# Optimization experiments

Measured on AMD Instinct MI355X. Metric: run time of the kernel, lower is better.

Reference implementation:

```python
import jax, jax.numpy as jnp
import numpy as np

B, C, P, H, W, S = 4, 256, 128, 56, 56, 5
EPS = 1e-5


def setup_inputs() -> dict:
    key = jax.random.key(0)
    ks = jax.random.split(key, 6)
    return {
        "x": jax.random.normal(ks[0], (B, C, H, W), jnp.float32),
        "Wt": jax.random.normal(ks[1], (P, C), jnp.float32) * 0.05,
        "Wp": jax.random.normal(ks[2], (P, C), jnp.float32) * 0.05,
        "Wg": jax.random.normal(ks[3], (S, P, C), jnp.float32) * 0.05,
        "W1": jax.random.normal(ks[4], (S, C, P), jnp.float32) * 0.05,
        "W2": jax.random.normal(ks[5], (S, C, P), jnp.float32) * 0.05,
        "gamma": jnp.ones((S, C), jnp.float32),
        "beta": jnp.zeros((S, C), jnp.float32),
    }


def _batchnorm(o, g, b):
    # training-mode BN over (batch, spatial); o: [b, C, n]
    mean = o.mean(axis=(0, 2), keepdims=True)
    var = ((o - mean) ** 2).mean(axis=(0, 2), keepdims=True)
    return (o - mean) * jax.lax.rsqrt(var + EPS) * g[None, :, None] + b[None, :, None]


def reference(x, Wt, Wp, Wg, W1, W2, gamma, beta):
    b, c, h, w = x.shape
    n = h * w
    xf = x.reshape(b, c, n)
    # 1x1 conv projections == channel matmuls
    t = jax.nn.relu(jnp.einsum('pc,bcn->bpn', Wt, xf))  # is_norm branch uses relu
    p = jax.nn.relu(jnp.einsum('pc,bcn->bpn', Wp, xf))
    att = jnp.einsum('bpi,bpj->bij', t, p)              # [b, n, n] affinity
    att = 0.5 * (att + jnp.swapaxes(att, 1, 2))         # is_sys symmetrization
    d = att.sum(axis=2)                                  # degree [b, n]
    d_safe = jnp.where(d != 0, d, 1.0)
    d_inv = jnp.where(d != 0, jax.lax.rsqrt(d_safe), 0.0)
    att = att * d_inv[:, None, :] * d_inv[:, :, None]    # D^-1/2 A D^-1/2
    out = xf
    for s in range(S):  # fixed small stage count
        g = jnp.einsum('pc,bcn->bpn', Wg[s], out)        # [b, P, n]
        ag = jnp.einsum('bij,bpj->bpi', att, g)          # att @ g over spatial
        o = jnp.einsum('cp,bpn->bcn', W1[s], ag) + jnp.einsum('cp,bpn->bcn', W2[s], g)
        out = _batchnorm(o, gamma[s], beta[s]) + out     # BN + residual
    return out.reshape(b, c, h, w)
```

## Files before the change

### kernel.cpp

```cpp
#include <hip/hip_runtime.h>

#define VMC(n) asm volatile("s_waitcnt vmcnt(" #n ")" ::: "memory")
#define LGKM0() asm volatile("s_waitcnt lgkmcnt(0)" ::: "memory")

namespace {

constexpr int Bc = 4;
constexpr int Cc = 256;
constexpr int Pc = 128;
constexpr int NcT = 3136;
constexpr int Np = 3200;
constexpr int Sc = 5;
constexpr int KSn = 5;
constexpr int KCH = 640;
constexpr float EPSc = 1e-5f;

typedef __attribute__((ext_vector_type(8))) short bf16x8;
typedef __attribute__((ext_vector_type(4))) float f32x4;
typedef __attribute__((ext_vector_type(8))) unsigned short u16x8;
typedef __attribute__((ext_vector_type(4))) unsigned short u16x4;

__device__ inline float bf2f(unsigned short u) {
    return __uint_as_float(((unsigned)u) << 16);
}
__device__ inline unsigned short f2bf(float f) {
    unsigned u = __float_as_uint(f);
    return (unsigned short)((u + 0x7FFFu + ((u >> 16) & 1u)) >> 16);
}

struct GP {
    const unsigned short* A; int lda; long aB; long aSl;
    const unsigned short* Bw; int ldb; long bB; long bSl;
    const unsigned short* A2; int lda2; long aB2;
    const unsigned short* B2; int ldb2; long bB2;
    int K; int K2; int nsl; int kchunk;
    unsigned short* outSM; int ldsm; long smB; long smSlice;
    unsigned short* outCM; long cmB;
    float* ps; float* ps2;
    const float* bnsc; const float* bnsh;
    const float* dinv;
    const unsigned short* oin;
    float* resid;
};

template <int MT, int EPI, int CMOUT, bool SPLITK, int BNSTAT, bool FUSEBN,
          bool XORM, bool DUALK>
__global__ __launch_bounds__(256) void mgemm(GP p)
{
    constexpr int TBA = MT * 64 * 2;
    constexpr int TBB = 128 * 64 * 2;
    constexpr int BUF = TBA + TBB;
    constexpr int OTB = MT * 132 * 4;
    constexpr int LDSZ = (4 * BUF > OTB + 2048) ? 4 * BUF : (OTB + 2048);
    __shared__ __align__(16) char lds[LDSZ];

    int b, kstart;
    long smOff;
    if (SPLITK) {
        b = blockIdx.z & 3;
        int ks = blockIdx.z >> 2;
        kstart = ks * p.kchunk;
        smOff = (long)ks * p.smSlice;
    } else {
        b = blockIdx.z; kstart = 0; smOff = 0;
    }
    const int n0 = blockIdx.x * 128;
    const int m0 = blockIdx.y * MT;
    const int tid = threadIdx.x;
    const int w = tid >> 6, l = tid & 63;

    const unsigned short* Ab = p.A + (size_t)b * p.aB + (size_t)m0 * p.lda;
    const unsigned short* Bb = p.Bw + (size_t)b * p.bB + (size_t)n0 * p.ldb;

    const int srow8 = tid >> 3;
    const int sgran = tid & 7;
    const int sswz = (sgran ^ (srow8 & 7)) * 8;
    constexpr int AR = MT / 32;

    constexpr int WC = (MT == 128) ? 2 : 4;
    constexpr int NB = 128 / WC / 16;
    const int wr = w / WC, wc = w % WC;

    f32x4 acc[4][NB] = {};

    float4 dvv[4];
    if constexpr (DUALK) {
#pragma unroll
        for (int r = 0; r < 4; ++r) {
            float4 v = *(const float4*)(p.dinv + (size_t)b * Np + m0 +
                                        wr * 64 + r * 16 + (l >> 4) * 4);
            v.x *= 0.5f; v.y *= 0.5f; v.z *= 0.5f; v.w *= 0.5f;
            dvv[r] = v;
        }
    }

    auto stage1 = [&](int buf, int sl, int k0) {
        char* base = lds + buf * BUF;
        const unsigned short* As = Ab + (size_t)sl * p.aSl + k0 + sswz;
#pragma unroll
        for (int j = 0; j < AR; ++j)
            __builtin_amdgcn_global_load_lds(
                (const __attribute__((address_space(1))) void*)
                    (As + (size_t)(j * 32 + srow8) * p.lda),
                (__attribute__((address_space(3))) void*)(base + j * 4096 + tid * 16),
                16, 0, 0);
        const unsigned short* Bs = Bb + (size_t)sl * p.bSl + k0 + sswz;
#pragma unroll
        for (int j = 0; j < 4; ++j)
            __builtin_amdgcn_global_load_lds(
                (const __attribute__((address_space(1))) void*)
                    (Bs + (size_t)(j * 32 + srow8) * p.ldb),
                (__attribute__((address_space(3))) void*)(base + TBA + j * 4096 + tid * 16),
                16, 0, 0);
    };

    auto stageB1 = [&](int buf, int k0) {
        char* base = lds + buf * BUF + TBA;
        const unsigned short* Bs = Bb + k0 + sswz;
#pragma unroll
        for (int j = 0; j < 4; ++j)
            __builtin_amdgcn_global_load_lds(
                (const __attribute__((address_space(1))) void*)
                    (Bs + (size_t)(j * 32 + srow8) * p.ldb),
                (__attribute__((address_space(3))) void*)(base + j * 4096 + tid * 16),
                16, 0, 0);
    };

    auto compute = [&](int buf) {
        const char* base = lds + buf * BUF;
        const int lo = l & 15, gq = l >> 4;
#pragma unroll
        for (int kh = 0; kh < 2; ++kh) {
            const int lg = kh * 4 + gq;
            bf16x8 bf[NB];
#pragma unroll
            for (int c = 0; c < NB; ++c) {
                int brow = wc * (16 * NB) + c * 16 + lo;
                bf[c] = *(const bf16x8*)(base + TBA + brow * 128 +
                                         ((lg ^ (brow & 7)) << 4));
            }
#pragma unroll
            for (int r = 0; r < 4; ++r) {
                int arow = wr * 64 + r * 16 + lo;
                bf16x8 af = *(const bf16x8*)(base + arow * 128 +
                                             ((lg ^ (arow & 7)) << 4));
#pragma unroll
                for (int c = 0; c < NB; ++c)
                    acc[r][c] = __builtin_amdgcn_mfma_f32_16x16x32_bf16(
                        af, bf[c], acc[r][c], 0, 0, 0);
            }
        }
    };

    if constexpr (FUSEBN) {
        struct FB {
            u16x8 ov[AR]; float4 r0[AR], r1[AR];
            float4 s0, s1, h0, h1; int k0;
        };
        FB fA, fB;
        auto fbIssue = [&](FB& f, int k0) {
            f.k0 = k0;
            f.s0 = *(const float4*)(p.bnsc + k0 + sgran * 8);
            f.s1 = *(const float4*)(p.bnsc + k0 + sgran * 8 + 4);
            f.h0 = *(const float4*)(p.bnsh + k0 + sgran * 8);
            f.h1 = *(const float4*)(p.bnsh + k0 + sgran * 8 + 4);
#pragma unroll
            for (int j = 0; j < AR; ++j) {
                size_t off = ((size_t)b * Np + (m0 + j * 32 + srow8)) * 256 +
                             k0 + sgran * 8;
                f.ov[j] = *(const u16x8*)(p.oin + off);
                f.r0[j] = *(const float4*)(p.resid + off);
                f.r1[j] = *(const float4*)(p.resid + off + 4);
            }
        };
        auto fbFin = [&](FB& f, int buf) {
            char* base = lds + buf * BUF;
#pragma unroll
            for (int j = 0; j < AR; ++j) {
                int row = j * 32 + srow8;
                int n = m0 + row;
                size_t off = ((size_t)b * Np + n) * 256 + f.k0 + sgran * 8;
                bool real = (n < NcT);
                float fu[8];
                fu[0] = real ? f.r0[j].x + fmaf(bf2f(f.ov[j][0]), f.s0.x, f.h0.x) : 0.f;
                fu[1] = real ? f.r0[j].y + fmaf(bf2f(f.ov[j][1]), f.s0.y, f.h0.y) : 0.f;
                fu[2] = real ? f.r0[j].z + fmaf(bf2f(f.ov[j][2]), f.s0.z, f.h0.z) : 0.f;
                fu[3] = real ? f.r0[j].w + fmaf(bf2f(f.ov[j][3]), f.s0.w, f.h0.w) : 0.f;
                fu[4] = real ? f.r1[j].x + fmaf(bf2f(f.ov[j][4]), f.s1.x, f.h1.x) : 0.f;
                fu[5] = real ? f.r1[j].y + fmaf(bf2f(f.ov[j][5]), f.s1.y, f.h1.y) : 0.f;
                fu[6] = real ? f.r1[j].z + fmaf(bf2f(f.ov[j][6]), f.s1.z, f.h1.z) : 0.f;
                fu[7] = real ? f.r1[j].w + fmaf(bf2f(f.ov[j][7]), f.s1.w, f.h1.w) : 0.f;
                float4 w0, w1;
                w0.x = fu[0]; w0.y = fu[1]; w0.z = fu[2]; w0.w = fu[3];
                w1.x = fu[4]; w1.y = fu[5]; w1.z = fu[6]; w1.w = fu[7];
                *(float4*)(p.resid + off) = w0;
                *(float4*)(p.resid + off + 4) = w1;
                u16x8 hv;
#pragma unroll
                for (int i = 0; i < 8; ++i) hv[i] = f2bf(fu[i]);
                *(u16x8*)(base + row * 128 + ((sgran ^ (row & 7)) << 4)) = hv;
            }
        };

        fbIssue(fA, kstart);        stageB1(0, kstart);
        fbIssue(fB, kstart + 64);   stageB1(1, kstart + 64);
        VMC(14);
        fbFin(fA, 0);
        fbIssue(fA, kstart + 128);  stageB1(2, kstart + 128);
        LGKM0();
        __builtin_amdgcn_s_barrier();
        __builtin_amdgcn_sched_barrier(0);
        compute(0);
        VMC(18);
        fbFin(fB, 1);
        fbIssue(fB, kstart + 192);  stageB1(3, kstart + 192);
        LGKM0();
        __builtin_amdgcn_s_barrier();
        __builtin_amdgcn_sched_barrier(0);
        compute(1);
        VMC(18);
        fbFin(fA, 2);
        LGKM0();
        __builtin_amdgcn_s_barrier();
        __builtin_amdgcn_sched_barrier(0);
        compute(2);
        VMC(4);
        fbFin(fB, 3);
        LGKM0();
        __builtin_amdgcn_s_barrier();
        __builtin_amdgcn_sched_barrier(0);
        compute(3);
        __syncthreads();
    } else {
        const int nsteps1 = (SPLITK ? p.kchunk : p.K) >> 6;
        const int spl2 = DUALK ? (p.K2 >> 6) : 0;
        const int loop1 = p.nsl * nsteps1;
        const int tot = loop1 + spl2;

        const unsigned short* Ab2 = DUALK ?
            (p.A2 + (size_t)b * p.aB2 + (size_t)m0 * p.lda2) : nullptr;
        const unsigned short* Bb2 = DUALK ?
            (p.B2 + (size_t)b * p.bB2 + (size_t)n0 * p.ldb2) : nullptr;
        auto stage2 = [&](int buf, int k0) {
            if constexpr (DUALK) {
                char* base = lds + buf * BUF;
                const unsigned short* As = Ab2 + k0 + sswz;
#pragma unroll
                for (int j = 0; j < AR; ++j)
                    __builtin_amdgcn_global_load_lds(
                        (const __attribute__((address_space(1))) void*)
                            (As + (size_t)(j * 32 + srow8) * p.lda2),
                        (__attribute__((address_space(3))) void*)(base + j * 4096 + tid * 16),
                        16, 0, 0);
                const unsigned short* Bs = Bb2 + k0 + sswz;
#pragma unroll
                for (int j = 0; j < 4; ++j)
                    __builtin_amdgcn_global_load_lds(
                        (const __attribute__((address_space(1))) void*)
                            (Bs + (size_t)(j * 32 + srow8) * p.ldb2),
                        (__attribute__((address_space(3))) void*)(base + TBA + j * 4096 + tid * 16),
                        16, 0, 0);
            }
        };

        auto stage_g = [&](int buf, int g) {
            if (g < loop1) {
                int sl = g / nsteps1;
                int st = g - sl * nsteps1;
                stage1(buf, sl, kstart + (st << 6));
            } else {
                stage2(buf, (g - loop1) << 6);
            }
        };

        stage_g(0, 0);
        if (1 < tot) stage_g(1, 1);
        if (2 < tot) stage_g(2, 2);
        for (int gs = 0; gs < tot; ++gs) {
            if constexpr (MT == 64) {
                if (gs + 2 < tot) VMC(12);
                else if (gs + 1 < tot) VMC(6);
                else VMC(0);
            } else {
                if (gs + 2 < tot) VMC(16);
                else if (gs + 1 < tot) VMC(8);
                else VMC(0);
            }
            __builtin_amdgcn_s_barrier();
            __builtin_amdgcn_sched_barrier(0);
            if (gs + 3 < tot) stage_g((gs + 3) & 3, gs + 3);
            compute(gs & 3);
            if constexpr (DUALK) {
                if (gs == loop1 - 1) {
#pragma unroll
                    for (int r = 0; r < 4; ++r) {
#pragma unroll
                        for (int c = 0; c < NB; ++c) {
                            acc[r][c][0] *= dvv[r].x;
                            acc[r][c][1] *= dvv[r].y;
                            acc[r][c][2] *= dvv[r].z;
                            acc[r][c][3] *= dvv[r].w;
                        }
                    }
                }
            }
        }
        __syncthreads();
    }

    float* ot = (float*)lds;
    {
        const int lo = l & 15, gq = l >> 4;
#pragma unroll
        for (int r = 0; r < 4; ++r)
#pragma unroll
            for (int c = 0; c < NB; ++c)
#pragma unroll
                for (int j = 0; j < 4; ++j) {
                    float v = acc[r][c][j];
                    if (EPI == 1) v = fmaxf(v, 0.f);
                    ot[(wr * 64 + r * 16 + gq * 4 + j) * 132 +
                       wc * (16 * NB) + c * 16 + lo] = v;
                }
    }
    __syncthreads();

    {
        constexpr int TPR = 256 / MT;
        const int r = tid / TPR;
        const int c0 = (tid % TPR) * (MT / 2);
        const int m0s = XORM ? (m0 ^ 128) : m0;
        unsigned short* dst = p.outSM + (size_t)b * p.smB + smOff +
                              (size_t)(m0s + r) * p.ldsm + n0 + c0;
#pragma unroll
        for (int k = 0; k < MT / 16; ++k) {
            u16x8 o;
#pragma unroll
            for (int j = 0; j < 8; ++j) o[j] = f2bf(ot[r * 132 + c0 + 8 * k + j]);
            *(u16x8*)(dst + 8 * k) = o;
        }
    }

    if (CMOUT) {
        const int c = tid >> 1, r0 = (tid & 1) * (MT / 2);
        const float* dv = p.dinv + (size_t)b * Np + m0 + r0;
        unsigned short* dst = p.outCM + (size_t)b * p.cmB +
                              (size_t)(n0 + c) * Np + m0 + r0;
#pragma unroll
        for (int k = 0; k < MT / 16; ++k) {
            u16x8 o;
#pragma unroll
            for (int j = 0; j < 8; ++j) {
                float v = ot[(r0 + 8 * k + j) * 132 + c];
                if (CMOUT == 2) v *= dv[8 * k + j];
                o[j] = f2bf(v);
            }
            *(u16x8*)(dst + 8 * k) = o;
        }
    }

    if (BNSTAT) {
        float* p1 = (float*)(lds + OTB);
        float* p2 = p1 + 256;
        const int col = tid & 127, half = tid >> 7;
        float s = 0.f, s2 = 0.f;
#pragma unroll
        for (int i = 0; i < MT / 2; ++i) {
            float v = ot[(half * (MT / 2) + i) * 132 + col];
            s += v;
            if (BNSTAT == 2) s2 = fmaf(v, v, s2);
        }
        p1[half * 128 + col] = s;
        if (BNSTAT == 2) p2[half * 128 + col] = s2;
        __syncthreads();
        if (tid < 128) {
            float aa = p1[tid] + p1[128 + tid];
            size_t slot = ((size_t)b * gridDim.y + blockIdx.y) * 256 + n0 + tid;
            p.ps[slot] = aa;
            if (BNSTAT == 2) p.ps2[slot] = p2[tid] + p2[128 + tid];
        }
    }
}

__global__ __launch_bounds__(256) void prep_k(
    const float* __restrict__ x, const float* __restrict__ Wt,
    const float* __restrict__ Wp, const float* __restrict__ Wg,
    const float* __restrict__ W1, const float* __restrict__ W2,
    unsigned short* __restrict__ Wcomb, unsigned short* __restrict__ Wgh,
    unsigned short* __restrict__ W1h, unsigned short* __restrict__ W2h,
    float* __restrict__ out_sm, unsigned short* __restrict__ outh)
{
    __shared__ float tb[64][65];
    int item = blockIdx.x;
    int t = threadIdx.x;
    if (item < 544) {
        size_t e = ((size_t)item * 256 + t) * 4;
        const float* src; unsigned short* dst;
        if (e < 32768)       { src = Wt + e;           dst = Wcomb + e; }
        else if (e < 65536)  { src = Wp + (e - 32768); dst = Wcomb + e; }
        else if (e < 229376) { size_t o = e - 65536;  src = Wg + o; dst = Wgh + o; }
        else if (e < 393216) { size_t o = e - 229376; src = W1 + o; dst = W1h + o; }
        else                 { size_t o = e - 393216; src = W2 + o; dst = W2h + o; }
        float4 v = *(const float4*)src;
        u16x4 t4;
        t4[0] = f2bf(v.x); t4[1] = f2bf(v.y); t4[2] = f2bf(v.z); t4[3] = f2bf(v.w);
        *(u16x4*)dst = t4;
        return;
    }
    int it = item - 544;
    int nx = it % 50, cy = (it / 50) % 4, b = it / 200;
    int c0 = cy * 64, n0 = nx * 64;
    const bool pad = (n0 >= NcT);
    if (!pad) {
        int ci = t >> 2, nb = (t & 3) * 16;
        const float* src = x + ((size_t)b * Cc + c0 + ci) * NcT + n0 + nb;
#pragma unroll
        for (int k = 0; k < 4; ++k) {
            float4 v = *(const float4*)(src + 4 * k);
            tb[ci][nb + 4 * k + 0] = v.x; tb[ci][nb + 4 * k + 1] = v.y;
            tb[ci][nb + 4 * k + 2] = v.z; tb[ci][nb + 4 * k + 3] = v.w;
        }
    }
    __syncthreads();
    int r = t >> 2, cb = (t & 3) * 16;
    size_t off = ((size_t)b * Np + n0 + r) * 256 + c0 + cb;
    float vv[16];
#pragma unroll
    for (int j = 0; j < 16; ++j) vv[j] = pad ? 0.f : tb[cb + j][r];
    float* dst = out_sm + off;
#pragma unroll
    for (int k = 0; k < 4; ++k) {
        float4 v; v.x = vv[4*k]; v.y = vv[4*k+1]; v.z = vv[4*k+2]; v.w = vv[4*k+3];
        *(float4*)(dst + 4 * k) = v;
    }
    u16x8 h1, h2;
#pragma unroll
    for (int j = 0; j < 8; ++j) { h1[j] = f2bf(vv[j]); h2[j] = f2bf(vv[8 + j]); }
    unsigned short* dh = outh + off;
    *(u16x8*)dh = h1;
    *(u16x8*)(dh + 8) = h2;
}

__global__ __launch_bounds__(256) void dinv_k(
    const unsigned short* __restrict__ U, const float* __restrict__ rp,
    float* __restrict__ dinv)
{
    __shared__ float rsl[256];
    int b = blockIdx.y, tid = threadIdx.x;
    float s = 0.f;
    for (int j = 0; j < 25; ++j) s += rp[((size_t)b * 25 + j) * 256 + tid];
    rsl[tid ^ 128] = s;
    __syncthreads();
    int i = blockIdx.x * 256 + tid;
    if (i < Np) {
        const unsigned short* row = U + ((size_t)b * Np + i) * 256;
        float acc = 0.f;
        for (int q0 = 0; q0 < 256; q0 += 8) {
            u16x8 v = *(const u16x8*)(row + q0);
#pragma unroll
            for (int j = 0; j < 8; ++j) acc = fmaf(bf2f(v[j]), rsl[q0 + j], acc);
        }
        float d = 0.5f * acc;
        dinv[(size_t)b * Np + i] = d > 0.f ? rsqrtf(d) : 0.f;
    }
}

__global__ __launch_bounds__(256) void bnfin_k(
    const float* __restrict__ ps, const float* __restrict__ ps2,
    const float* __restrict__ gamma, const float* __restrict__ beta,
    float* __restrict__ scale, float* __restrict__ shift)
{
    __shared__ float l1[256], l2[256];
    int t = threadIdx.x;
    int c = blockIdx.x * 16 + (t & 15);
    int gl = t >> 4;
    float a = 0.f, a2 = 0.f;
    for (int g = gl; g < 100; g += 16) {
        a += ps[(size_t)g * 256 + c];
        a2 += ps2[(size_t)g * 256 + c];
    }
    l1[t] = a; l2[t] = a2;
    __syncthreads();
    if (gl == 0) {
#pragma unroll
        for (int j = 1; j < 16; ++j) {
            a += l1[j * 16 + (t & 15)];
            a2 += l2[j * 16 + (t & 15)];
        }
        const float inv = 1.f / (float)(Bc * NcT);
        float mean = a * inv;
        float var = a2 * inv - mean * mean;
        float sc = gamma[c] * rsqrtf(var + EPSc);
        scale[c] = sc;
        shift[c] = beta[c] - mean * sc;
    }
}

__global__ __launch_bounds__(256) void xpoutbn_k(
    const float* __restrict__ out_sm, const unsigned short* __restrict__ oin,
    const float* __restrict__ scale, const float* __restrict__ shift,
    float* __restrict__ outp)
{
    __shared__ float tb[64][65];
    __shared__ float lsc[64], lsh[64];
    int b = blockIdx.z, c0 = blockIdx.y * 64, n0 = blockIdx.x * 64;
    int t = threadIdx.x;
    if (t < 64) { lsc[t] = scale[c0 + t]; lsh[t] = shift[c0 + t]; }
    __syncthreads();
    {
        int r = t >> 2, cb = (t & 3) * 16;
        size_t off = ((size_t)b * Np + n0 + r) * 256 + c0 + cb;
#pragma unroll
        for (int k = 0; k < 2; ++k) {
            float4 a0 = *(const float4*)(out_sm + off + 8 * k);
            float4 a1 = *(const float4*)(out_sm + off + 8 * k + 4);
            u16x8 ov = *(const u16x8*)(oin + off + 8 * k);
            tb[r][cb + 8*k + 0] = a0.x + fmaf(bf2f(ov[0]), lsc[cb + 8*k + 0], lsh[cb + 8*k + 0]);
            tb[r][cb + 8*k + 1] = a0.y + fmaf(bf2f(ov[1]), lsc[cb + 8*k + 1], lsh[cb + 8*k + 1]);
            tb[r][cb + 8*k + 2] = a0.z + fmaf(bf2f(ov[2]), lsc[cb + 8*k + 2], lsh[cb + 8*k + 2]);
            tb[r][cb + 8*k + 3] = a0.w + fmaf(bf2f(ov[3]), lsc[cb + 8*k + 3], lsh[cb + 8*k + 3]);
            tb[r][cb + 8*k + 4] = a1.x + fmaf(bf2f(ov[4]), lsc[cb + 8*k + 4], lsh[cb + 8*k + 4]);
            tb[r][cb + 8*k + 5] = a1.y + fmaf(bf2f(ov[5]), lsc[cb + 8*k + 5], lsh[cb + 8*k + 5]);
            tb[r][cb + 8*k + 6] = a1.z + fmaf(bf2f(ov[6]), lsc[cb + 8*k + 6], lsh[cb + 8*k + 6]);
            tb[r][cb + 8*k + 7] = a1.w + fmaf(bf2f(ov[7]), lsc[cb + 8*k + 7], lsh[cb + 8*k + 7]);
        }
    }
    __syncthreads();
    {
        int c = t >> 2, rb = (t & 3) * 16;
        float vv[16];
#pragma unroll
        for (int j = 0; j < 16; ++j) vv[j] = tb[rb + j][c];
        float* dst = outp + ((size_t)b * Cc + c0 + c) * NcT + n0 + rb;
#pragma unroll
        for (int k = 0; k < 4; ++k) {
            float4 v; v.x = vv[4*k]; v.y = vv[4*k+1]; v.z = vv[4*k+2]; v.w = vv[4*k+3];
            *(float4*)(dst + 4 * k) = v;
        }
    }
}

}

extern "C" void kernel_launch(void* const* d_in, const int* in_sizes, int n_in,
                              void* d_out, int out_size, void* d_ws, size_t ws_size,
                              hipStream_t stream) {
    const float* x     = (const float*)d_in[0];
    const float* Wt    = (const float*)d_in[1];
    const float* Wp    = (const float*)d_in[2];
    const float* Wg    = (const float*)d_in[3];
    const float* W1    = (const float*)d_in[4];
    const float* W2    = (const float*)d_in[5];
    const float* gamma = (const float*)d_in[6];
    const float* beta  = (const float*)d_in[7];

    char* p = (char*)d_ws;
    auto alloc = [&](size_t bytes) { char* r = p; p += (bytes + 255) & ~(size_t)255; return r; };
    float*          out_sm = (float*)         alloc((size_t)Bc * Np * 256 * 4);
    unsigned short* outh   = (unsigned short*)alloc((size_t)Bc * Np * 256 * 2);
    unsigned short* U_sm   = (unsigned short*)alloc((size_t)Bc * Np * 256 * 2);
    unsigned short* U_cm   = (unsigned short*)alloc((size_t)Bc * 256 * Np * 2);
    unsigned short* g_sm   = (unsigned short*)alloc((size_t)Bc * Np * Pc * 2);
    unsigned short* g_cmd  = (unsigned short*)alloc((size_t)Bc * Pc * Np * 2);
    unsigned short* o_sm   = (unsigned short*)alloc((size_t)Bc * Np * 256 * 2);
    unsigned short* Cpart  = (unsigned short*)alloc((size_t)KSn * Bc * 256 * Pc * 2);
    unsigned short* WMb    = (unsigned short*)alloc((size_t)Bc * Cc * 256 * 2);
    unsigned short* Wcomb  = (unsigned short*)alloc((size_t)Cc * Cc * 2);
    unsigned short* Wgh    = (unsigned short*)alloc((size_t)Sc * Pc * Cc * 2);
    unsigned short* W1h    = (unsigned short*)alloc((size_t)Sc * Cc * Pc * 2);
    unsigned short* W2h    = (unsigned short*)alloc((size_t)Sc * Cc * Pc * 2);
    float*          rp     = (float*)         alloc((size_t)100 * 256 * 4);
    float*          dinv   = (float*)         alloc((size_t)Bc * Np * 4);
    float*          ps     = (float*)         alloc((size_t)100 * 256 * 4);
    float*          ps2    = (float*)         alloc((size_t)100 * 256 * 4);
    float*          scale  = (float*)         alloc(256 * 4);
    float*          shiftb = (float*)         alloc(256 * 4);

    const long NpC = (long)Np * 256;
    dim3 blk(256);

    prep_k<<<1344, blk, 0, stream>>>(x, Wt, Wp, Wg, W1, W2,
                                     Wcomb, Wgh, W1h, W2h, out_sm, outh);

    {
        GP g{};
        g.A = outh; g.lda = 256; g.aB = NpC; g.aSl = 0;
        g.Bw = Wcomb; g.ldb = 256; g.bB = 0; g.bSl = 0;
        g.K = 256; g.nsl = 1;
        g.outSM = U_sm; g.ldsm = 256; g.smB = NpC; g.smSlice = 0;
        g.outCM = U_cm; g.cmB = (long)256 * Np;
        g.ps = rp;
        mgemm<128, 1, 1, false, 1, false, false, false>
            <<<dim3(2, 25, Bc), blk, 0, stream>>>(g);
    }

    dinv_k<<<dim3(13, Bc), blk, 0, stream>>>(U_sm, rp, dinv);

    for (int s = 0; s < Sc; ++s) {
        {
            GP g{};
            g.A = outh; g.lda = 256; g.aB = NpC; g.aSl = 0;
            g.Bw = Wgh + (size_t)s * Pc * Cc; g.ldb = 256; g.bB = 0; g.bSl = 0;
            g.K = 256; g.nsl = 1;
            g.outSM = g_sm; g.ldsm = 128; g.smB = (long)Np * 128; g.smSlice = 0;
            g.outCM = g_cmd; g.cmB = (long)Pc * Np;
            g.dinv = dinv;
            g.oin = o_sm; g.bnsc = scale; g.bnsh = shiftb; g.resid = out_sm;
            if (s == 0)
                mgemm<64, 0, 2, false, 0, false, false, false>
                    <<<dim3(1, 50, Bc), blk, 0, stream>>>(g);
            else
                mgemm<64, 0, 2, false, 0, true, false, false>
                    <<<dim3(1, 50, Bc), blk, 0, stream>>>(g);
        }
        {
            GP g{};
            g.A = U_cm; g.lda = Np; g.aB = (long)256 * Np; g.aSl = 0;
            g.Bw = g_cmd; g.ldb = Np; g.bB = (long)Pc * Np; g.bSl = 0;
            g.K = Np; g.kchunk = KCH; g.nsl = 1;
            g.outSM = Cpart; g.ldsm = 128; g.smB = (long)256 * Pc;
            g.smSlice = (long)Bc * 256 * Pc;
            mgemm<64, 0, 0, true, 0, false, true, false>
                <<<dim3(1, 4, KSn * Bc), blk, 0, stream>>>(g);
        }
        {
            GP g{};
            g.A = W1h + (size_t)s * Cc * Pc; g.lda = 128; g.aB = 0; g.aSl = 0;
            g.Bw = Cpart; g.ldb = 128; g.bB = (long)256 * Pc;
            g.bSl = (long)Bc * 256 * Pc;
            g.K = 128; g.nsl = KSn;
            g.outSM = WMb; g.ldsm = 256; g.smB = (long)Cc * 256; g.smSlice = 0;
            mgemm<64, 0, 0, false, 0, false, false, false>
                <<<dim3(2, 4, Bc), blk, 0, stream>>>(g);
        }
        {
            GP g{};
            g.A = U_sm; g.lda = 256; g.aB = NpC; g.aSl = 0;
            g.Bw = WMb; g.ldb = 256; g.bB = (long)Cc * 256; g.bSl = 0;
            g.K = 256; g.nsl = 1;
            g.A2 = g_sm; g.lda2 = 128; g.aB2 = (long)Np * 128;
            g.B2 = W2h + (size_t)s * Cc * Pc; g.ldb2 = 128; g.bB2 = 0;
            g.K2 = 128;
            g.outSM = o_sm; g.ldsm = 256; g.smB = NpC; g.smSlice = 0;
            g.ps = ps; g.ps2 = ps2;
            g.dinv = dinv;
            mgemm<128, 0, 0, false, 2, false, false, true>
                <<<dim3(2, 25, Bc), blk, 0, stream>>>(g);
        }
        bnfin_k<<<16, blk, 0, stream>>>(ps, ps2, gamma + s * Cc, beta + s * Cc,
                                        scale, shiftb);
    }

    xpoutbn_k<<<dim3(49, 4, Bc), blk, 0, stream>>>(out_sm, o_sm, scale, shiftb,
                                                   (float*)d_out);
}
```

Before: 250.5 us.

## Fuse per-stage GEMM chain into one persistent kernel with atomic flag barriers

The five per-stage launches (g projection, split-K att·g, W1 mix, dual-K output GEMM, BN finalize) are replaced by one 200-block kernel per stage. The GEMM bodies become device functions that take explicit block indices, and phases are ordered by global atomic counters with release/acquire semantics and sleep-polling. The aim is to remove launch gaps and tail drain between the dependent GEMMs. The cost is spin-wait latency and a 128 KB LDS footprint that allows only one block per CU. The scheme also depends on all 200 blocks being co-resident; a bounded spin guard avoids hangs but could silently break ordering if it ever trips.

```diff
diff --git a/kernel.cpp b/kernel.cpp
--- a/kernel.cpp
+++ b/kernel.cpp
@@ -43,29 +43,44 @@
     float* resid;
 };
 
+__device__ inline void signal_flag(unsigned* f) {
+    __syncthreads();
+    if (threadIdx.x == 0)
+        __hip_atomic_fetch_add(f, 1u, __ATOMIC_RELEASE, __HIP_MEMORY_SCOPE_AGENT);
+}
+__device__ inline void wait_flag(unsigned* f, unsigned target) {
+    if (threadIdx.x == 0) {
+        int guard = 0;
+        while (__hip_atomic_load(f, __ATOMIC_ACQUIRE,
+                                 __HIP_MEMORY_SCOPE_AGENT) < target) {
+            __builtin_amdgcn_s_sleep(8);
+            if (++guard > (1 << 20)) break;
+        }
+    }
+    __syncthreads();
+}
+
 template <int MT, int EPI, int CMOUT, bool SPLITK, int BNSTAT, bool FUSEBN,
           bool XORM, bool DUALK>
-__global__ __launch_bounds__(256) void mgemm(GP p)
+__device__ void gemm_body(char* lds, int bx, int by, int bz, int MY, const GP& p)
 {
     constexpr int TBA = MT * 64 * 2;
     constexpr int TBB = 128 * 64 * 2;
     constexpr int BUF = TBA + TBB;
     constexpr int OTB = MT * 132 * 4;
-    constexpr int LDSZ = (4 * BUF > OTB + 2048) ? 4 * BUF : (OTB + 2048);
-    __shared__ __align__(16) char lds[LDSZ];
 
     int b, kstart;
     long smOff;
     if (SPLITK) {
-        b = blockIdx.z & 3;
-        int ks = blockIdx.z >> 2;
+        b = bz & 3;
+        int ks = bz >> 2;
         kstart = ks * p.kchunk;
         smOff = (long)ks * p.smSlice;
     } else {
-        b = blockIdx.z; kstart = 0; smOff = 0;
-    }
-    const int n0 = blockIdx.x * 128;
-    const int m0 = blockIdx.y * MT;
+        b = bz; kstart = 0; smOff = 0;
+    }
+    const int n0 = bx * 128;
+    const int m0 = by * MT;
     const int tid = threadIdx.x;
     const int w = tid >> 6, l = tid & 63;
 
@@ -375,10 +390,100 @@
         __syncthreads();
         if (tid < 128) {
             float aa = p1[tid] + p1[128 + tid];
-            size_t slot = ((size_t)b * gridDim.y + blockIdx.y) * 256 + n0 + tid;
+            size_t slot = ((size_t)b * MY + by) * 256 + n0 + tid;
             p.ps[slot] = aa;
             if (BNSTAT == 2) p.ps2[slot] = p2[tid] + p2[128 + tid];
         }
+    }
+    __syncthreads();
+}
+
+__device__ void bnfin_body(char* ldsb, int bid,
+                           const float* __restrict__ ps,
+                           const float* __restrict__ ps2,
+                           const float* __restrict__ gamma,
+                           const float* __restrict__ beta,
+                           float* __restrict__ scale, float* __restrict__ shift)
+{
+    float* l1 = (float*)ldsb;
+    float* l2 = l1 + 256;
+    int t = threadIdx.x;
+    int c = bid * 16 + (t & 15);
+    int gl = t >> 4;
+    float a = 0.f, a2 = 0.f;
+    for (int g = gl; g < 100; g += 16) {
+        a += ps[(size_t)g * 256 + c];
+        a2 += ps2[(size_t)g * 256 + c];
+    }
+    l1[t] = a; l2[t] = a2;
+    __syncthreads();
+    if (gl == 0) {
+#pragma unroll
+        for (int j = 1; j < 16; ++j) {
+            a += l1[j * 16 + (t & 15)];
+            a2 += l2[j * 16 + (t & 15)];
+        }
+        const float inv = 1.f / (float)(Bc * NcT);
+        float mean = a * inv;
+        float var = a2 * inv - mean * mean;
+        float sc = gamma[c] * rsqrtf(var + EPSc);
+        scale[c] = sc;
+        shift[c] = beta[c] - mean * sc;
+    }
+}
+
+template <int MT, int EPI, int CMOUT, bool SPLITK, int BNSTAT, bool FUSEBN,
+          bool XORM, bool DUALK>
+__global__ __launch_bounds__(256) void mgemm_g(GP p)
+{
+    constexpr int TBA = MT * 64 * 2;
+    constexpr int BUF = TBA + 128 * 64 * 2;
+    constexpr int OTB = MT * 132 * 4;
+    constexpr int LDSZ = (4 * BUF > OTB + 2048) ? 4 * BUF : (OTB + 2048);
+    __shared__ __align__(16) char lds[LDSZ];
+    gemm_body<MT, EPI, CMOUT, SPLITK, BNSTAT, FUSEBN, XORM, DUALK>(
+        lds, blockIdx.x, blockIdx.y, blockIdx.z, (int)gridDim.y, p);
+}
+
+struct SP {
+    GP g, abt, wm, o;
+    const float* ps; const float* ps2;
+    const float* gammap; const float* betap;
+    float* scale; float* shiftb;
+    unsigned* flags;
+};
+
+template <bool FIRST>
+__global__ __launch_bounds__(256) void stage_k(SP sp)
+{
+    __shared__ __align__(16) char lds[131072];
+    const int bid = blockIdx.x;
+
+    gemm_body<64, 0, 2, false, 0, (FIRST ? false : true), false, false>(
+        lds, 0, bid % 50, bid / 50, 50, sp.g);
+    signal_flag(&sp.flags[0]);
+
+    if (bid < 80) {
+        wait_flag(&sp.flags[0], 200);
+        gemm_body<64, 0, 0, true, 0, false, true, false>(
+            lds, 0, bid % 4, bid / 4, 4, sp.abt);
+        signal_flag(&sp.flags[1]);
+    }
+    if (bid < 32) {
+        wait_flag(&sp.flags[1], 80);
+        gemm_body<64, 0, 0, false, 0, false, false, false>(
+            lds, bid % 2, (bid / 2) % 4, bid / 8, 4, sp.wm);
+        signal_flag(&sp.flags[2]);
+    }
+    wait_flag(&sp.flags[2], 32);
+    gemm_body<128, 0, 0, false, 2, false, false, true>(
+        lds, bid % 2, (bid / 2) % 25, bid / 50, 25, sp.o);
+    signal_flag(&sp.flags[3]);
+
+    if (bid < 16) {
+        wait_flag(&sp.flags[3], 200);
+        bnfin_body(lds, bid, sp.ps, sp.ps2, sp.gammap, sp.betap,
+                   sp.scale, sp.shiftb);
     }
 }
 
@@ -465,37 +570,6 @@
     }
 }
 
-__global__ __launch_bounds__(256) void bnfin_k(
-    const float* __restrict__ ps, const float* __restrict__ ps2,
-    const float* __restrict__ gamma, const float* __restrict__ beta,
-    float* __restrict__ scale, float* __restrict__ shift)
-{
-    __shared__ float l1[256], l2[256];
-    int t = threadIdx.x;
-    int c = blockIdx.x * 16 + (t & 15);
-    int gl = t >> 4;
-    float a = 0.f, a2 = 0.f;
-    for (int g = gl; g < 100; g += 16) {
-        a += ps[(size_t)g * 256 + c];
-        a2 += ps2[(size_t)g * 256 + c];
-    }
-    l1[t] = a; l2[t] = a2;
-    __syncthreads();
-    if (gl == 0) {
-#pragma unroll
-        for (int j = 1; j < 16; ++j) {
-            a += l1[j * 16 + (t & 15)];
-            a2 += l2[j * 16 + (t & 15)];
-        }
-        const float inv = 1.f / (float)(Bc * NcT);
-        float mean = a * inv;
-        float var = a2 * inv - mean * mean;
-        float sc = gamma[c] * rsqrtf(var + EPSc);
-        scale[c] = sc;
-        shift[c] = beta[c] - mean * sc;
-    }
-}
-
 __global__ __launch_bounds__(256) void xpoutbn_k(
     const float* __restrict__ out_sm, const unsigned short* __restrict__ oin,
     const float* __restrict__ scale, const float* __restrict__ shift,
@@ -575,9 +649,12 @@
     float*          ps2    = (float*)         alloc((size_t)100 * 256 * 4);
     float*          scale  = (float*)         alloc(256 * 4);
     float*          shiftb = (float*)         alloc(256 * 4);
+    unsigned*       flags  = (unsigned*)      alloc(Sc * 4 * sizeof(unsigned));
 
     const long NpC = (long)Np * 256;
     dim3 blk(256);
+
+    hipMemsetAsync(flags, 0, Sc * 4 * sizeof(unsigned), stream);
 
     prep_k<<<1344, blk, 0, stream>>>(x, Wt, Wp, Wg, W1, W2,
                                      Wcomb, Wgh, W1h, W2h, out_sm, outh);
@@ -590,65 +667,48 @@
         g.outSM = U_sm; g.ldsm = 256; g.smB = NpC; g.smSlice = 0;
         g.outCM = U_cm; g.cmB = (long)256 * Np;
         g.ps = rp;
-        mgemm<128, 1, 1, false, 1, false, false, false>
+        mgemm_g<128, 1, 1, false, 1, false, false, false>
             <<<dim3(2, 25, Bc), blk, 0, stream>>>(g);
     }
 
     dinv_k<<<dim3(13, Bc), blk, 0, stream>>>(U_sm, rp, dinv);
 
     for (int s = 0; s < Sc; ++s) {
-        {
-            GP g{};
-            g.A = outh; g.lda = 256; g.aB = NpC; g.aSl = 0;
-            g.Bw = Wgh + (size_t)s * Pc * Cc; g.ldb = 256; g.bB = 0; g.bSl = 0;
-            g.K = 256; g.nsl = 1;
-            g.outSM = g_sm; g.ldsm = 128; g.smB = (long)Np * 128; g.smSlice = 0;
-            g.outCM = g_cmd; g.cmB = (long)Pc * Np;
-            g.dinv = dinv;
-            g.oin = o_sm; g.bnsc = scale; g.bnsh = shiftb; g.resid = out_sm;
-            if (s == 0)
-                mgemm<64, 0, 2, false, 0, false, false, false>
-                    <<<dim3(1, 50, Bc), blk, 0, stream>>>(g);
-            else
-                mgemm<64, 0, 2, false, 0, true, false, false>
-                    <<<dim3(1, 50, Bc), blk, 0, stream>>>(g);
-        }
-        {
-            GP g{};
-            g.A = U_cm; g.lda = Np; g.aB = (long)256 * Np; g.aSl = 0;
-            g.Bw = g_cmd; g.ldb = Np; g.bB = (long)Pc * Np; g.bSl = 0;
-            g.K = Np; g.kchunk = KCH; g.nsl = 1;
-            g.outSM = Cpart; g.ldsm = 128; g.smB = (long)256 * Pc;
-            g.smSlice = (long)Bc * 256 * Pc;
-            mgemm<64, 0, 0, true, 0, false, true, false>
-                <<<dim3(1, 4, KSn * Bc), blk, 0, stream>>>(g);
-        }
-        {
-            GP g{};
-            g.A = W1h + (size_t)s * Cc * Pc; g.lda = 128; g.aB = 0; g.aSl = 0;
-            g.Bw = Cpart; g.ldb = 128; g.bB = (long)256 * Pc;
-            g.bSl = (long)Bc * 256 * Pc;
-            g.K = 128; g.nsl = KSn;
-            g.outSM = WMb; g.ldsm = 256; g.smB = (long)Cc * 256; g.smSlice = 0;
-            mgemm<64, 0, 0, false, 0, false, false, false>
-                <<<dim3(2, 4, Bc), blk, 0, stream>>>(g);
-        }
-        {
-            GP g{};
-            g.A = U_sm; g.lda = 256; g.aB = NpC; g.aSl = 0;
-            g.Bw = WMb; g.ldb = 256; g.bB = (long)Cc * 256; g.bSl = 0;
-            g.K = 256; g.nsl = 1;
-            g.A2 = g_sm; g.lda2 = 128; g.aB2 = (long)Np * 128;
-            g.B2 = W2h + (size_t)s * Cc * Pc; g.ldb2 = 128; g.bB2 = 0;
-            g.K2 = 128;
-            g.outSM = o_sm; g.ldsm = 256; g.smB = NpC; g.smSlice = 0;
-            g.ps = ps; g.ps2 = ps2;
-            g.dinv = dinv;
-            mgemm<128, 0, 0, false, 2, false, false, true>
-                <<<dim3(2, 25, Bc), blk, 0, stream>>>(g);
-        }
-        bnfin_k<<<16, blk, 0, stream>>>(ps, ps2, gamma + s * Cc, beta + s * Cc,
-                                        scale, shiftb);
+        SP sp{};
+        sp.g.A = outh; sp.g.lda = 256; sp.g.aB = NpC; sp.g.aSl = 0;
+        sp.g.Bw = Wgh + (size_t)s * Pc * Cc; sp.g.ldb = 256; sp.g.bB = 0; sp.g.bSl = 0;
+        sp.g.K = 256; sp.g.nsl = 1;
+        sp.g.outSM = g_sm; sp.g.ldsm = 128; sp.g.smB = (long)Np * 128; sp.g.smSlice = 0;
+        sp.g.outCM = g_cmd; sp.g.cmB = (long)Pc * Np;
+        sp.g.dinv = dinv;
+        sp.g.oin = o_sm; sp.g.bnsc = scale; sp.g.bnsh = shiftb; sp.g.resid = out_sm;
+        sp.abt.A = U_cm; sp.abt.lda = Np; sp.abt.aB = (long)256 * Np; sp.abt.aSl = 0;
+        sp.abt.Bw = g_cmd; sp.abt.ldb = Np; sp.abt.bB = (long)Pc * Np; sp.abt.bSl = 0;
+        sp.abt.K = Np; sp.abt.kchunk = KCH; sp.abt.nsl = 1;
+        sp.abt.outSM = Cpart; sp.abt.ldsm = 128; sp.abt.smB = (long)256 * Pc;
+        sp.abt.smSlice = (long)Bc * 256 * Pc;
+        sp.wm.A = W1h + (size_t)s * Cc * Pc; sp.wm.lda = 128; sp.wm.aB = 0; sp.wm.aSl = 0;
+        sp.wm.Bw = Cpart; sp.wm.ldb = 128; sp.wm.bB = (long)256 * Pc;
+        sp.wm.bSl = (long)Bc * 256 * Pc;
+        sp.wm.K = 128; sp.wm.nsl = KSn;
+        sp.wm.outSM = WMb; sp.wm.ldsm = 256; sp.wm.smB = (long)Cc * 256; sp.wm.smSlice = 0;
+        sp.o.A = U_sm; sp.o.lda = 256; sp.o.aB = NpC; sp.o.aSl = 0;
+        sp.o.Bw = WMb; sp.o.ldb = 256; sp.o.bB = (long)Cc * 256; sp.o.bSl = 0;
+        sp.o.K = 256; sp.o.nsl = 1;
+        sp.o.A2 = g_sm; sp.o.lda2 = 128; sp.o.aB2 = (long)Np * 128;
+        sp.o.B2 = W2h + (size_t)s * Cc * Pc; sp.o.ldb2 = 128; sp.o.bB2 = 0;
+        sp.o.K2 = 128;
+        sp.o.outSM = o_sm; sp.o.ldsm = 256; sp.o.smB = NpC; sp.o.smSlice = 0;
+        sp.o.ps = ps; sp.o.ps2 = ps2;
+        sp.o.dinv = dinv;
+        sp.ps = ps; sp.ps2 = ps2;
+        sp.gammap = gamma + (size_t)s * Cc;
+        sp.betap = beta + (size_t)s * Cc;
+        sp.scale = scale; sp.shiftb = shiftb;
+        sp.flags = flags + s * 4;
+
+        if (s == 0) stage_k<true><<<200, blk, 0, stream>>>(sp);
+        else        stage_k<false><<<200, blk, 0, stream>>>(sp);
     }
 
     xpoutbn_k<<<dim3(49, 4, Bc), blk, 0, stream>>>(out_sm, o_sm, scale, shiftb,
```

Measured after the change: 508.5 us. 103% more time.
